# Kernel tuning notes

Measured on AMD Instinct MI355X. Metric: run time of the kernel, lower is better.

Reference implementation:

```python
import jax, jax.numpy as jnp
import numpy as np

N_NODES = 100000
N_EDGES = 1600000
N_REL = 8
N_HEADS = 4
IN_FEAT = 128
OUT_FEAT = 64
D_HEAD = OUT_FEAT // N_HEADS
LEAKY_SLOPE = 0.2


def setup_inputs() -> dict:
    key = jax.random.key(0)
    ks = jax.random.split(key, 8)
    inputs = jax.random.normal(ks[0], (N_NODES, IN_FEAT), dtype=jnp.float32)
    conv_weights = jax.random.normal(ks[1], (N_REL, N_HEADS, IN_FEAT, D_HEAD), dtype=jnp.float32) * (1.0 / np.sqrt(IN_FEAT))
    attn_l = jax.random.normal(ks[2], (N_REL, N_HEADS, D_HEAD), dtype=jnp.float32) * (1.0 / np.sqrt(D_HEAD))
    attn_r = jax.random.normal(ks[3], (N_REL, N_HEADS, D_HEAD), dtype=jnp.float32) * (1.0 / np.sqrt(D_HEAD))
    h_bias = jax.random.normal(ks[4], (OUT_FEAT,), dtype=jnp.float32)
    src_idx = jax.random.randint(ks[5], (N_EDGES,), 0, N_NODES, dtype=jnp.int64) if jax.config.jax_enable_x64 else jax.random.randint(ks[5], (N_EDGES,), 0, N_NODES, dtype=jnp.int32)
    dst_idx = jax.random.randint(ks[6], (N_EDGES,), 0, N_NODES, dtype=src_idx.dtype)
    rel_idx = jax.random.randint(ks[7], (N_EDGES,), 0, N_REL, dtype=src_idx.dtype)
    return {"inputs": inputs, "conv_weights": conv_weights, "attn_l": attn_l,
            "attn_r": attn_r, "h_bias": h_bias, "src_idx": src_idx,
            "dst_idx": dst_idx, "rel_idx": rel_idx}


def reference(inputs, conv_weights, attn_l, attn_r, h_bias, src_idx, dst_idx, rel_idx):
    N = inputs.shape[0]
    # Per-node per-relation projection: [N, R, H, Dh]
    # (equivalent math to the per-relation grouped matmul over unique nodes)
    proj = jnp.einsum('ni,rhid->nrhd', inputs, conv_weights)
    # Gather per-edge src/dst projected features under the edge's relation: [E, H, Dh]
    feat_src = proj[src_idx, rel_idx]
    feat_dst = proj[dst_idx, rel_idx]
    # Attention logits per edge/head: [E, H]
    el = jnp.sum(feat_src * attn_l[rel_idx], axis=-1)
    er = jnp.sum(feat_dst * attn_r[rel_idx], axis=-1)
    score = jax.nn.leaky_relu(el + er, negative_slope=LEAKY_SLOPE)
    # Edge softmax over incoming edges of each destination node (per head)
    smax = jax.ops.segment_max(score, dst_idx, num_segments=N)        # [N, H]
    e = jnp.exp(score - smax[dst_idx])                                # [E, H]
    denom = jax.ops.segment_sum(e, dst_idx, num_segments=N)          # [N, H]
    alpha = e / denom[dst_idx]                                        # [E, H]
    # Weighted aggregation of src features to dst nodes: [N, H, Dh]
    h = jax.ops.segment_sum(alpha[..., None] * feat_src, dst_idx, num_segments=N)
    h = h.reshape(N, OUT_FEAT) + h_bias
    return h
```

## Files before the change

### kernel.cpp

```cpp
#include <hip/hip_runtime.h>
#include <hip/hip_bf16.h>


#define NN 100000
#define NNP 100096
#define NE 1600000
#define NH 4
#define INF_ 128
#define DH 16
#define NCOL 576
#define LEAKY 0.2f
#define NBUCK 391
#define BSHIFT 8
#define CHUNK 4096
#define CAP 5120
#define GEMM_BLOCKS 782

typedef __hip_bfloat16 bf16;
typedef __attribute__((ext_vector_type(8))) short bf16x8;
typedef __attribute__((ext_vector_type(4))) short bf16x4;
typedef __attribute__((ext_vector_type(4))) float f32x4;

static __device__ __forceinline__ short f2bs(float x) {
    bf16 b = __float2bfloat16(x);
    return *reinterpret_cast<short*>(&b);
}
static __device__ __forceinline__ float bflo(unsigned u) { return __uint_as_float(u << 16); }
static __device__ __forceinline__ float bfhi(unsigned u) { return __uint_as_float(u & 0xffff0000u); }

__global__ void build_wextT(const float* __restrict__ W, const float* __restrict__ al,
                            const float* __restrict__ ar, short* __restrict__ wxt2,
                            int* __restrict__ gCursor) {
    if (blockIdx.x >= 288) {
        int i = (blockIdx.x - 288) * 256 + threadIdx.x;
        if (i < NBUCK) gCursor[i] = 0;
        return;
    }
    int idx = blockIdx.x * 256 + threadIdx.x;
    int e = idx & 7, lane = (idx >> 3) & 63, ct = (idx >> 9) & 3, ks = (idx >> 11) & 3, cb = idx >> 13;
    int g = lane >> 4, r = lane & 15;
    int c = cb * 64 + ct * 16 + r;
    int k = ks * 32 + g * 8 + e;
    float v;
    if (c < 512) {
        int rr = c >> 6, rem = c & 63, h = rem >> 4, d = rem & 15;
        v = W[((rr * NH + h) * INF_ + k) * DH + d];
    } else {
        int rh = c - 512;
        const float* a = al;
        if (rh >= 32) { rh -= 32; a = ar; }
        int rr = rh >> 2, h = rh & 3;
        const float* wp = &W[((rr * NH + h) * INF_ + k) * DH];
        const float* ap = &a[(rr * NH + h) * DH];
        float s = 0.f;
        #pragma unroll
        for (int d = 0; d < DH; ++d) s += wp[d] * ap[d];
        v = s;
    }
    wxt2[idx] = f2bs(v);
}

__global__ __launch_bounds__(256) void gemm_fused(
    const float* __restrict__ A, const short* __restrict__ WxT2,
    bf16* __restrict__ projR, float* __restrict__ elr,
    const int* __restrict__ src, const int* __restrict__ dst, const int* __restrict__ rel,
    int* __restrict__ gCursor, int* __restrict__ pairbuf) {
    __shared__ short As[16384];
    int t = threadIdx.x;

    if (blockIdx.x >= GEMM_BLOCKS) {
        int* hist = (int*)As;
        int blk = blockIdx.x - GEMM_BLOCKS;
        for (int i = t; i < NBUCK; i += 256) hist[i] = 0;
        __syncthreads();
        int base = blk * CHUNK;
        #pragma unroll
        for (int j = 0; j < CHUNK / 256; ++j) {
            int e = base + j * 256 + t;
            if (e < NE) atomicAdd(&hist[dst[e] >> BSHIFT], 1);
        }
        __syncthreads();
        for (int i = t; i < NBUCK; i += 256) {
            int v = hist[i];
            hist[i] = v ? (i * CAP + atomicAdd(&gCursor[i], v)) : 0;
        }
        __syncthreads();
        #pragma unroll
        for (int j = 0; j < CHUNK / 256; ++j) {
            int e = base + j * 256 + t;
            if (e < NE) {
                int d = dst[e];
                int b = d >> BSHIFT;
                int rec = ((d & 255) << 20) | (src[e] * 8 + rel[e]);
                int pos = atomicAdd(&hist[b], 1);
                pairbuf[pos] = rec;
            }
        }
        return;
    }

    int wv = t >> 6, lane = t & 63;
    int n0 = blockIdx.x * 128;
    int g = lane >> 4, r = lane & 15;

    #pragma unroll
    for (int j = 0; j < 8; ++j) {
        int i = j * 256 + t;
        int row = i >> 4, c8 = i & 15;
        int gr = n0 + row;
        bf16x8 v;
        if (gr < NN) {
            float4 f0 = *(const float4*)&A[gr * INF_ + c8 * 8];
            float4 f1 = *(const float4*)&A[gr * INF_ + c8 * 8 + 4];
            v[0] = f2bs(f0.x); v[1] = f2bs(f0.y); v[2] = f2bs(f0.z); v[3] = f2bs(f0.w);
            v[4] = f2bs(f1.x); v[5] = f2bs(f1.y); v[6] = f2bs(f1.z); v[7] = f2bs(f1.w);
        } else {
            v = (bf16x8)(short)0;
        }
        *(bf16x8*)&As[(row * 16 + (c8 ^ (row & 7))) * 8] = v;
    }
    __syncthreads();

    bf16x8 afr[2][4];
    #pragma unroll
    for (int nt = 0; nt < 2; ++nt) {
        int row = wv * 32 + nt * 16 + r;
        #pragma unroll
        for (int ks = 0; ks < 4; ++ks)
            afr[nt][ks] = *(const bf16x8*)&As[(row * 16 + ((ks * 4 + g) ^ (r & 7))) * 8];
    }
    __syncthreads();
    short* Csh = &As[wv * 4096];
    float* Csf = (float*)Csh;
    int n0w = n0 + wv * 32;

    for (int cb = 0; cb < 9; ++cb) {
        f32x4 acc[2][4] = {};
        #pragma unroll
        for (int ks = 0; ks < 4; ++ks) {
            #pragma unroll
            for (int ct = 0; ct < 4; ++ct) {
                bf16x8 b = *(const bf16x8*)&WxT2[(((cb * 4 + ks) * 4 + ct) * 64 + lane) * 8];
                acc[0][ct] = __builtin_amdgcn_mfma_f32_16x16x32_bf16(b, afr[0][ks], acc[0][ct], 0, 0, 0);
                acc[1][ct] = __builtin_amdgcn_mfma_f32_16x16x32_bf16(b, afr[1][ks], acc[1][ct], 0, 0, 0);
            }
        }
        if (cb < 8) {
            #pragma unroll
            for (int nt = 0; nt < 2; ++nt) {
                int rr = nt * 16 + r;
                #pragma unroll
                for (int ct = 0; ct < 4; ++ct) {
                    bf16x4 p;
                    p[0] = f2bs(acc[nt][ct][0]); p[1] = f2bs(acc[nt][ct][1]);
                    p[2] = f2bs(acc[nt][ct][2]); p[3] = f2bs(acc[nt][ct][3]);
                    *(bf16x4*)&Csh[rr * 64 + (((ct * 4 + g) ^ ((rr & 7) << 1)) << 2)] = p;
                }
            }
            __builtin_amdgcn_wave_barrier();
            size_t base = ((size_t)cb * NN + n0w) * 64;
            #pragma unroll
            for (int q = 0; q < 4; ++q) {
                int rr = (lane >> 3) + q * 8;
                if (n0w + rr < NN) {
                    bf16x8 vv = *(const bf16x8*)&Csh[rr * 64 + (((lane & 7) ^ (rr & 7)) << 3)];
                    __builtin_nontemporal_store(vv, (bf16x8*)&((short*)projR)[base + q * 512 + lane * 8]);
                }
            }
            __builtin_amdgcn_wave_barrier();
        } else {
            #pragma unroll
            for (int nt = 0; nt < 2; ++nt) {
                int rr = nt * 16 + r;
                #pragma unroll
                for (int ct = 0; ct < 4; ++ct)
                    *(f32x4*)&Csf[rr * 64 + (((ct * 4 + g) ^ ((rr & 7) << 1)) << 2)] = acc[nt][ct];
            }
            __builtin_amdgcn_wave_barrier();
            #pragma unroll
            for (int q = 0; q < 8; ++q) {
                int rr = (lane >> 4) + q * 4;
                if (n0w + rr < NN) {
                    f32x4 vv = *(const f32x4*)&Csf[rr * 64 + (((lane & 15) ^ ((rr & 7) << 1)) << 2)];
                    __builtin_nontemporal_store(vv, (f32x4*)&elr[(size_t)n0w * 64 + q * 256 + lane * 4]);
                }
            }
        }
    }
}

__global__ __launch_bounds__(256) void exact_place(
    const int* __restrict__ gCursor, const int* __restrict__ pairbuf,
    int2* __restrict__ offdeg, int2* __restrict__ rec2) {
    __shared__ int hist[256];
    __shared__ int tsum[256];
    int b = blockIdx.x, t = threadIdx.x;
    int start = b * CAP, cnt = gCursor[b];
    hist[t] = 0;
    __syncthreads();
    for (int i = t; i < cnt; i += 256) atomicAdd(&hist[pairbuf[start + i] >> 20], 1);
    __syncthreads();
    int own = hist[t];
    tsum[t] = own;
    __syncthreads();
    for (int st = 1; st < 256; st <<= 1) {
        int y = (t >= st) ? tsum[t - st] : 0;
        __syncthreads();
        tsum[t] += y;
        __syncthreads();
    }
    int excl = start + tsum[t] - own;
    int node = b * 256 + t;
    if (node < NN) offdeg[node] = make_int2(excl, own);
    __syncthreads();
    hist[t] = excl;
    __syncthreads();
    for (int i = t; i < cnt; i += 256) {
        int rec = pairbuf[start + i];
        int pos = atomicAdd(&hist[rec >> 20], 1);
        int sr = rec & 0xFFFFF;
        rec2[pos] = make_int2((sr >> 3) * 64 + (sr & 7) * 4,
                              (sr & 7) * (NN * 64) + (sr >> 3) * 64);
    }
}

__global__ __launch_bounds__(256) void agg(
    const int2* __restrict__ offdeg, const int2* __restrict__ rec2,
    const float* __restrict__ elr, const bf16* __restrict__ projR,
    const float* __restrict__ bias, float* __restrict__ out) {
    __shared__ float s_alpha[4][64][4];
    __shared__ int   s_pidx[4][64];
    __shared__ float s_er[4][32];
    int wv = threadIdx.x >> 6, lane = threadIdx.x & 63;
    int d = blockIdx.x * 4 + wv;
    if (d >= NN) return;
    int2 od = offdeg[d];
    int off = od.x, deg = od.y;
    int end = off + deg;

    if (lane < 32) s_er[wv][lane] = elr[d * 64 + 32 + lane];
    __builtin_amdgcn_wave_barrier();
    asm volatile("s_waitcnt lgkmcnt(0)" ::: "memory");

    if (deg == 0) {
        if (lane < 32) {
            float2 bb = *(const float2*)&bias[lane * 2];
            *(float2*)&out[d * 64 + lane * 2] = bb;
        }
    } else if (deg <= 64) {
        int i = off + lane;
        float e0 = 0.f, e1 = 0.f, e2 = 0.f, e3 = 0.f;
        int pidx = 0;
        if (i < end) {
            int2 rv = rec2[i];
            pidx = rv.y;
            float4 el4 = *(const float4*)&elr[rv.x];
            int erb = rv.x & 63;
            float x;
            x = el4.x + s_er[wv][erb + 0]; x = x > 0.f ? x : LEAKY * x; e0 = __expf(x);
            x = el4.y + s_er[wv][erb + 1]; x = x > 0.f ? x : LEAKY * x; e1 = __expf(x);
            x = el4.z + s_er[wv][erb + 2]; x = x > 0.f ? x : LEAKY * x; e2 = __expf(x);
            x = el4.w + s_er[wv][erb + 3]; x = x > 0.f ? x : LEAKY * x; e3 = __expf(x);
        }
        s_pidx[wv][lane] = pidx;
        *(float4*)&s_alpha[wv][lane][0] = make_float4(e0, e1, e2, e3);
        __builtin_amdgcn_wave_barrier();
        asm volatile("s_waitcnt lgkmcnt(0)" ::: "memory");

        int col2 = (lane & 31) * 2;
        int hl = lane >> 5;
        int h2 = (lane & 31) >> 3;
        float acc0 = 0.f, acc1 = 0.f, dsum = 0.f;
        int j = 0;
        for (; j + 8 <= deg; j += 8) {
            unsigned uu[4];
            #pragma unroll
            for (int p = 0; p < 4; ++p) {
                int myp = s_pidx[wv][j + 2 * p + hl];
                uu[p] = *(const unsigned*)&projR[myp + col2];
            }
            #pragma unroll
            for (int p = 0; p < 4; ++p) {
                float a_self = s_alpha[wv][j + 2 * p + hl][h2];
                float a_oth  = s_alpha[wv][j + 2 * p + 1 - hl][h2];
                unsigned uo = __shfl_xor((int)uu[p], 32);
                acc0 = fmaf(a_self, bflo(uu[p]), acc0);
                acc1 = fmaf(a_self, bfhi(uu[p]), acc1);
                acc0 = fmaf(a_oth, bflo(uo), acc0);
                acc1 = fmaf(a_oth, bfhi(uo), acc1);
                dsum += a_self + a_oth;
            }
        }
        for (; j + 2 <= deg; j += 2) {
            int myp = s_pidx[wv][j + hl];
            unsigned u = *(const unsigned*)&projR[myp + col2];
            float a_self = s_alpha[wv][j + hl][h2];
            float a_oth  = s_alpha[wv][j + 1 - hl][h2];
            unsigned uo = __shfl_xor((int)u, 32);
            acc0 = fmaf(a_self, bflo(u), acc0);
            acc1 = fmaf(a_self, bfhi(u), acc1);
            acc0 = fmaf(a_oth, bflo(uo), acc0);
            acc1 = fmaf(a_oth, bfhi(uo), acc1);
            dsum += a_self + a_oth;
        }
        if (j < deg) {
            int myp = s_pidx[wv][j];
            unsigned u = *(const unsigned*)&projR[myp + col2];
            float a = s_alpha[wv][j][h2];
            acc0 = fmaf(a, bflo(u), acc0);
            acc1 = fmaf(a, bfhi(u), acc1);
            dsum += a;
        }
        if (lane < 32) {
            float inv = 1.0f / dsum;
            float2 bb = *(const float2*)&bias[col2];
            float2 o;
            o.x = acc0 * inv + bb.x;
            o.y = acc1 * inv + bb.y;
            *(float2*)&out[d * 64 + col2] = o;
        }
    } else {
        int c = lane, h = c >> 4;
        float dsum0 = 0.f, dsum1 = 0.f, dsum2 = 0.f, dsum3 = 0.f;
        for (int i = off + lane; i < end; i += 64) {
            int2 rv = rec2[i];
            float4 el4 = *(const float4*)&elr[rv.x];
            int erb = rv.x & 63;
            float x;
            x = el4.x + s_er[wv][erb + 0]; x = x > 0.f ? x : LEAKY * x; dsum0 += __expf(x);
            x = el4.y + s_er[wv][erb + 1]; x = x > 0.f ? x : LEAKY * x; dsum1 += __expf(x);
            x = el4.z + s_er[wv][erb + 2]; x = x > 0.f ? x : LEAKY * x; dsum2 += __expf(x);
            x = el4.w + s_er[wv][erb + 3]; x = x > 0.f ? x : LEAKY * x; dsum3 += __expf(x);
        }
        #pragma unroll
        for (int m = 32; m; m >>= 1) {
            dsum0 += __shfl_xor(dsum0, m, 64);
            dsum1 += __shfl_xor(dsum1, m, 64);
            dsum2 += __shfl_xor(dsum2, m, 64);
            dsum3 += __shfl_xor(dsum3, m, 64);
        }
        float dh = (h == 0) ? dsum0 : (h == 1) ? dsum1 : (h == 2) ? dsum2 : dsum3;
        float rd = 1.0f / dh;
        float acc = 0.f;
        for (int i = off; i < end; ++i) {
            int2 rv = rec2[i];
            float x = elr[rv.x + h] + s_er[wv][(rv.x & 63) + h];
            x = x > 0.f ? x : LEAKY * x;
            acc = fmaf(__expf(x) * rd, __bfloat162float(projR[rv.y + c]), acc);
        }
        out[d * 64 + c] = acc + bias[c];
    }
}

extern "C" void kernel_launch(void* const* d_in, const int* in_sizes, int n_in,
                              void* d_out, int out_size, void* d_ws, size_t ws_size,
                              hipStream_t stream) {
    const float* inputs = (const float*)d_in[0];
    const float* convw  = (const float*)d_in[1];
    const float* attn_l = (const float*)d_in[2];
    const float* attn_r = (const float*)d_in[3];
    const float* h_bias = (const float*)d_in[4];
    const int*   src    = (const int*)d_in[5];
    const int*   dst    = (const int*)d_in[6];
    const int*   rel    = (const int*)d_in[7];
    float* out = (float*)d_out;

    char* ws = (char*)d_ws;
    size_t o = 0;
    bf16* projR = (bf16*)(ws + o);  o += 102400000ull;
    float* elr  = (float*)(ws + o); o += 25600000ull;
    short* wxt2 = (short*)(ws + o); o += 147456;
    int2* offdeg = (int2*)(ws + o); o += 800768;
    int* gCursor = (int*)(ws + o);  o += 2048;
    int* pairbuf = (int*)(ws + o);  o += (size_t)NBUCK * CAP * 4;
    int2* rec2   = (int2*)(ws + o); o += (size_t)NBUCK * CAP * 8;

    hipLaunchKernelGGL(build_wextT, dim3(290), dim3(256), 0, stream, convw, attn_l, attn_r, wxt2, gCursor);
    hipLaunchKernelGGL(gemm_fused, dim3(GEMM_BLOCKS + NBUCK), dim3(256), 0, stream,
                       inputs, wxt2, projR, elr, src, dst, rel, gCursor, pairbuf);
    hipLaunchKernelGGL(exact_place, dim3(NBUCK), dim3(256), 0, stream, gCursor, pairbuf, offdeg, rec2);
    hipLaunchKernelGGL(agg, dim3(25000), dim3(256), 0, stream, offdeg, rec2, elr, projR, h_bias, out);
}
```

Measured before the change: 150.7 us.

## Move edge bucketing into weight-build kernel and stage GEMM B tiles in LDS

Moves the edge histogram/scatter blocks out of the GEMM kernel and into the weight-preparation kernel, so the scatter runs alongside the small weight build instead of the GEMM. The gCursor reset now uses a memset. In the GEMM, each column block of the extended weight matrix is loaded cooperatively into shared memory, with the next block prefetched into registers. All waves then read B from LDS instead of each wave re-reading it from global memory. This adds extra LDS (16KB), two block barriers per column block, and a memset launch.

```diff
diff --git a/kernel.cpp b/kernel.cpp
--- a/kernel.cpp
+++ b/kernel.cpp
@@ -14,7 +14,7 @@
 #define BSHIFT 8
 #define CHUNK 4096
 #define CAP 5120
-#define GEMM_BLOCKS 782
+#define WEXT_BLOCKS 288
 
 typedef __hip_bfloat16 bf16;
 typedef __attribute__((ext_vector_type(8))) short bf16x8;
@@ -28,15 +28,45 @@
 static __device__ __forceinline__ float bflo(unsigned u) { return __uint_as_float(u << 16); }
 static __device__ __forceinline__ float bfhi(unsigned u) { return __uint_as_float(u & 0xffff0000u); }
 
-__global__ void build_wextT(const float* __restrict__ W, const float* __restrict__ al,
-                            const float* __restrict__ ar, short* __restrict__ wxt2,
-                            int* __restrict__ gCursor) {
-    if (blockIdx.x >= 288) {
-        int i = (blockIdx.x - 288) * 256 + threadIdx.x;
-        if (i < NBUCK) gCursor[i] = 0;
+__global__ __launch_bounds__(256) void wext_scatter(
+    const float* __restrict__ W, const float* __restrict__ al, const float* __restrict__ ar,
+    short* __restrict__ wxt2,
+    const int* __restrict__ src, const int* __restrict__ dst, const int* __restrict__ rel,
+    int* __restrict__ gCursor, int* __restrict__ pairbuf) {
+    __shared__ int hist[NBUCK];
+    int t = threadIdx.x;
+
+    if (blockIdx.x >= WEXT_BLOCKS) {
+        int blk = blockIdx.x - WEXT_BLOCKS;
+        for (int i = t; i < NBUCK; i += 256) hist[i] = 0;
+        __syncthreads();
+        int base = blk * CHUNK;
+        #pragma unroll
+        for (int j = 0; j < CHUNK / 256; ++j) {
+            int e = base + j * 256 + t;
+            if (e < NE) atomicAdd(&hist[dst[e] >> BSHIFT], 1);
+        }
+        __syncthreads();
+        for (int i = t; i < NBUCK; i += 256) {
+            int v = hist[i];
+            hist[i] = v ? (i * CAP + atomicAdd(&gCursor[i], v)) : 0;
+        }
+        __syncthreads();
+        #pragma unroll
+        for (int j = 0; j < CHUNK / 256; ++j) {
+            int e = base + j * 256 + t;
+            if (e < NE) {
+                int d = dst[e];
+                int b = d >> BSHIFT;
+                int rec = ((d & 255) << 20) | (src[e] * 8 + rel[e]);
+                int pos = atomicAdd(&hist[b], 1);
+                pairbuf[pos] = rec;
+            }
+        }
         return;
     }
-    int idx = blockIdx.x * 256 + threadIdx.x;
+
+    int idx = blockIdx.x * 256 + t;
     int e = idx & 7, lane = (idx >> 3) & 63, ct = (idx >> 9) & 3, ks = (idx >> 11) & 3, cb = idx >> 13;
     int g = lane >> 4, r = lane & 15;
     int c = cb * 64 + ct * 16 + r;
@@ -60,45 +90,12 @@
     wxt2[idx] = f2bs(v);
 }
 
-__global__ __launch_bounds__(256) void gemm_fused(
+__global__ __launch_bounds__(256) void gemm_direct(
     const float* __restrict__ A, const short* __restrict__ WxT2,
-    bf16* __restrict__ projR, float* __restrict__ elr,
-    const int* __restrict__ src, const int* __restrict__ dst, const int* __restrict__ rel,
-    int* __restrict__ gCursor, int* __restrict__ pairbuf) {
+    bf16* __restrict__ projR, float* __restrict__ elr) {
     __shared__ short As[16384];
+    __shared__ short Bs[8192];
     int t = threadIdx.x;
-
-    if (blockIdx.x >= GEMM_BLOCKS) {
-        int* hist = (int*)As;
-        int blk = blockIdx.x - GEMM_BLOCKS;
-        for (int i = t; i < NBUCK; i += 256) hist[i] = 0;
-        __syncthreads();
-        int base = blk * CHUNK;
-        #pragma unroll
-        for (int j = 0; j < CHUNK / 256; ++j) {
-            int e = base + j * 256 + t;
-            if (e < NE) atomicAdd(&hist[dst[e] >> BSHIFT], 1);
-        }
-        __syncthreads();
-        for (int i = t; i < NBUCK; i += 256) {
-            int v = hist[i];
-            hist[i] = v ? (i * CAP + atomicAdd(&gCursor[i], v)) : 0;
-        }
-        __syncthreads();
-        #pragma unroll
-        for (int j = 0; j < CHUNK / 256; ++j) {
-            int e = base + j * 256 + t;
-            if (e < NE) {
-                int d = dst[e];
-                int b = d >> BSHIFT;
-                int rec = ((d & 255) << 20) | (src[e] * 8 + rel[e]);
-                int pos = atomicAdd(&hist[b], 1);
-                pairbuf[pos] = rec;
-            }
-        }
-        return;
-    }
-
     int wv = t >> 6, lane = t & 63;
     int n0 = blockIdx.x * 128;
     int g = lane >> 4, r = lane & 15;
@@ -119,6 +116,10 @@
         }
         *(bf16x8*)&As[(row * 16 + (c8 ^ (row & 7))) * 8] = v;
     }
+    bf16x8 breg[4];
+    #pragma unroll
+    for (int q = 0; q < 4; ++q)
+        breg[q] = *(const bf16x8*)&WxT2[(q * 256 + t) * 8];
     __syncthreads();
 
     bf16x8 afr[2][4];
@@ -135,12 +136,22 @@
     int n0w = n0 + wv * 32;
 
     for (int cb = 0; cb < 9; ++cb) {
+        #pragma unroll
+        for (int q = 0; q < 4; ++q)
+            *(bf16x8*)&Bs[(q * 256 + t) * 8] = breg[q];
+        __syncthreads();
+        if (cb < 8) {
+            #pragma unroll
+            for (int q = 0; q < 4; ++q)
+                breg[q] = *(const bf16x8*)&WxT2[((cb + 1) * 1024 + q * 256 + t) * 8];
+        }
+
         f32x4 acc[2][4] = {};
         #pragma unroll
         for (int ks = 0; ks < 4; ++ks) {
             #pragma unroll
             for (int ct = 0; ct < 4; ++ct) {
-                bf16x8 b = *(const bf16x8*)&WxT2[(((cb * 4 + ks) * 4 + ct) * 64 + lane) * 8];
+                bf16x8 b = *(const bf16x8*)&Bs[((ks * 4 + ct) * 64 + lane) * 8];
                 acc[0][ct] = __builtin_amdgcn_mfma_f32_16x16x32_bf16(b, afr[0][ks], acc[0][ct], 0, 0, 0);
                 acc[1][ct] = __builtin_amdgcn_mfma_f32_16x16x32_bf16(b, afr[1][ks], acc[1][ct], 0, 0, 0);
             }
@@ -186,6 +197,7 @@
                 }
             }
         }
+        __syncthreads();
     }
 }
 
@@ -375,9 +387,10 @@
     int* pairbuf = (int*)(ws + o);  o += (size_t)NBUCK * CAP * 4;
     int2* rec2   = (int2*)(ws + o); o += (size_t)NBUCK * CAP * 8;
 
-    hipLaunchKernelGGL(build_wextT, dim3(290), dim3(256), 0, stream, convw, attn_l, attn_r, wxt2, gCursor);
-    hipLaunchKernelGGL(gemm_fused, dim3(GEMM_BLOCKS + NBUCK), dim3(256), 0, stream,
-                       inputs, wxt2, projR, elr, src, dst, rel, gCursor, pairbuf);
+    hipMemsetAsync(gCursor, 0, NBUCK * sizeof(int), stream);
+    hipLaunchKernelGGL(wext_scatter, dim3(WEXT_BLOCKS + NBUCK), dim3(256), 0, stream,
+                       convw, attn_l, attn_r, wxt2, src, dst, rel, gCursor, pairbuf);
+    hipLaunchKernelGGL(gemm_direct, dim3(NNP / 128), dim3(256), 0, stream, inputs, wxt2, projR, elr);
     hipLaunchKernelGGL(exact_place, dim3(NBUCK), dim3(256), 0, stream, gCursor, pairbuf, offdeg, rec2);
     hipLaunchKernelGGL(agg, dim3(25000), dim3(256), 0, stream, offdeg, rec2, elr, projR, h_bias, out);
 }
```

Measured after the change: 166.9 us. 10.7% more time.
